# Performance work log

Measured on AMD Instinct MI355X. Metric: run time of the kernel, lower is better.

The kernel has to match this reference:

```python
import jax, jax.numpy as jnp
import numpy as np


def setup_inputs() -> dict:
    key = jax.random.key(0)
    k1, k2 = jax.random.split(key)
    B, N, C = 2, 8192, 32
    coords = jax.random.randint(k1, (B, N, 3), 0, 100, dtype=jnp.int32)
    features = jax.random.normal(k2, (B, N, C), dtype=jnp.float32)
    return {"coords": coords, "features": features, "len_batch": B}


def _detection_score(c, f):
    # c: [N,3] int32 coords, f: [N,C] float features
    f = jax.nn.relu(f)
    # beta: per-row normalization by row max
    beta = f / jnp.max(f, axis=1, keepdims=True)
    # pairwise squared distances via the exact integer expansion
    # ||a-b||^2 = |a|^2 + |b|^2 - 2 a.b  (exact in int32 for coords < 100,
    # and identical to the original's int16 arithmetic since no overflow)
    sq = jnp.sum(c * c, axis=1)                       # [N]
    d2 = sq[:, None] + sq[None, :] - 2 * (c @ c.T)    # [N,N] int32
    dist = jnp.sqrt(d2.astype(jnp.float32))           # [N,N]
    # topk(k=1, largest=False) == argmin (self-distance 0 -> nearest is self)
    nn_idx = jnp.argmin(dist, axis=1)                 # [N]
    # faithful to original: feature[neighbors,:][0] selects only row 0's
    # nearest neighbor's feature, shape [C]
    neighbor_feat = f[nn_idx[0]]                      # [C]
    alpha = jnp.exp(f) / jnp.exp(neighbor_feat)[None, :]
    gamma = jnp.max(alpha * beta, axis=1)             # [N]
    return gamma / jnp.linalg.norm(gamma)


def reference(coords, features, len_batch):
    # original concatenates per-batch scores along dim 0
    scores = jax.vmap(_detection_score)(coords, features)  # [B,N]
    return scores.reshape(-1)
```

## Files before the change

kernel.cpp:

```cpp
#include <hip/hip_runtime.h>


constexpr int kN = 8192;
constexpr int kC = 32;

__global__ __launch_bounds__(256) void gamma_kernel(const float* __restrict__ feats,
                                                    float* __restrict__ out,
                                                    float* __restrict__ sumsq) {
    const int b   = blockIdx.y;
    const int row = blockIdx.x * 256 + threadIdx.x;
    const float* fb = feats + (size_t)b * kN * kC;

    const float4* fr = reinterpret_cast<const float4*>(fb + (size_t)row * kC);
    const float4* f0 = reinterpret_cast<const float4*>(fb);

    float v[kC], r0[kC];
#pragma unroll
    for (int q = 0; q < kC / 4; ++q) {
        float4 t = fr[q];
        v[4 * q + 0] = fmaxf(t.x, 0.f);
        v[4 * q + 1] = fmaxf(t.y, 0.f);
        v[4 * q + 2] = fmaxf(t.z, 0.f);
        v[4 * q + 3] = fmaxf(t.w, 0.f);
        float4 z = f0[q];
        r0[4 * q + 0] = fmaxf(z.x, 0.f);
        r0[4 * q + 1] = fmaxf(z.y, 0.f);
        r0[4 * q + 2] = fmaxf(z.z, 0.f);
        r0[4 * q + 3] = fmaxf(z.w, 0.f);
    }

    float m = 0.f;
#pragma unroll
    for (int j = 0; j < kC; ++j) m = fmaxf(m, v[j]);
    const float inv_m = 1.0f / m;

    float g = 0.f;
#pragma unroll
    for (int j = 0; j < kC; ++j) {
        g = fmaxf(g, __expf(v[j] - r0[j]) * (v[j] * inv_m));
    }

    out[(size_t)b * kN + row] = g;

    float ss = g * g;
#pragma unroll
    for (int off = 32; off > 0; off >>= 1) ss += __shfl_down(ss, off, 64);
    if ((threadIdx.x & 63) == 0) atomicAdd(&sumsq[b], ss);
}

__global__ __launch_bounds__(256) void norm_kernel(float* __restrict__ out,
                                                   const float* __restrict__ sumsq) {
    const int i = blockIdx.x * 256 + threadIdx.x;
    const int b = i >> 13;
    out[i] = out[i] / sqrtf(sumsq[b]);
}

extern "C" void kernel_launch(void* const* d_in, const int* in_sizes, int n_in,
                              void* d_out, int out_size, void* d_ws, size_t ws_size,
                              hipStream_t stream) {
    const float* feats = (const float*)d_in[1];
    float* out = (float*)d_out;
    float* sumsq = (float*)d_ws;

    const int B = out_size / kN;

    hipMemsetAsync(sumsq, 0, (size_t)B * sizeof(float), stream);

    dim3 grid1(kN / 256, B);
    gamma_kernel<<<grid1, 256, 0, stream>>>(feats, out, sumsq);

    const int total = B * kN;
    norm_kernel<<<total / 256, 256, 0, stream>>>(out, sumsq);
}
```

Measured before the change: 64.68 us.

## Fuse gamma and normalization into one cooperative kernel with grid sync

```diff
diff --git a/kernel.cpp b/kernel.cpp
--- a/kernel.cpp
+++ b/kernel.cpp
@@ -1,74 +1,89 @@
 #include <hip/hip_runtime.h>
+#include <hip/hip_cooperative_groups.h>
+
+namespace cg = cooperative_groups;
 
 
 constexpr int kN = 8192;
 constexpr int kC = 32;
+constexpr int kBlock = 256;
+constexpr int kBlocksPerBatch = kN / kBlock;
 
-__global__ __launch_bounds__(256) void gamma_kernel(const float* __restrict__ feats,
-                                                    float* __restrict__ out,
-                                                    float* __restrict__ sumsq) {
-    const int b   = blockIdx.y;
-    const int row = blockIdx.x * 256 + threadIdx.x;
-    const float* fb = feats + (size_t)b * kN * kC;
+__global__ __launch_bounds__(kBlock) void detection_kernel(
+    const float* __restrict__ feats, float* __restrict__ out,
+    float* __restrict__ partials) {
+  cg::grid_group grid = cg::this_grid();
 
-    const float4* fr = reinterpret_cast<const float4*>(fb + (size_t)row * kC);
-    const float4* f0 = reinterpret_cast<const float4*>(fb);
+  const int blk = blockIdx.x;
+  const int b = blk / kBlocksPerBatch;
+  const int row = (blk % kBlocksPerBatch) * kBlock + threadIdx.x;
+  const float* fb = feats + (size_t)b * kN * kC;
 
-    float v[kC], r0[kC];
+  const float4* fr = reinterpret_cast<const float4*>(fb + (size_t)row * kC);
+  const float4* f0 = reinterpret_cast<const float4*>(fb);
+
+  float v[kC], r0[kC];
 #pragma unroll
-    for (int q = 0; q < kC / 4; ++q) {
-        float4 t = fr[q];
-        v[4 * q + 0] = fmaxf(t.x, 0.f);
-        v[4 * q + 1] = fmaxf(t.y, 0.f);
-        v[4 * q + 2] = fmaxf(t.z, 0.f);
-        v[4 * q + 3] = fmaxf(t.w, 0.f);
-        float4 z = f0[q];
-        r0[4 * q + 0] = fmaxf(z.x, 0.f);
-        r0[4 * q + 1] = fmaxf(z.y, 0.f);
-        r0[4 * q + 2] = fmaxf(z.z, 0.f);
-        r0[4 * q + 3] = fmaxf(z.w, 0.f);
-    }
+  for (int q = 0; q < kC / 4; ++q) {
+    float4 t = fr[q];
+    v[4 * q + 0] = fmaxf(t.x, 0.f);
+    v[4 * q + 1] = fmaxf(t.y, 0.f);
+    v[4 * q + 2] = fmaxf(t.z, 0.f);
+    v[4 * q + 3] = fmaxf(t.w, 0.f);
+    float4 z = f0[q];
+    r0[4 * q + 0] = fmaxf(z.x, 0.f);
+    r0[4 * q + 1] = fmaxf(z.y, 0.f);
+    r0[4 * q + 2] = fmaxf(z.z, 0.f);
+    r0[4 * q + 3] = fmaxf(z.w, 0.f);
+  }
 
-    float m = 0.f;
+  float m = 0.f;
 #pragma unroll
-    for (int j = 0; j < kC; ++j) m = fmaxf(m, v[j]);
-    const float inv_m = 1.0f / m;
+  for (int j = 0; j < kC; ++j) m = fmaxf(m, v[j]);
+  const float inv_m = 1.0f / m;
 
-    float g = 0.f;
+  float g = 0.f;
 #pragma unroll
-    for (int j = 0; j < kC; ++j) {
-        g = fmaxf(g, __expf(v[j] - r0[j]) * (v[j] * inv_m));
-    }
+  for (int j = 0; j < kC; ++j)
+    g = fmaxf(g, __expf(v[j] - r0[j]) * (v[j] * inv_m));
 
-    out[(size_t)b * kN + row] = g;
+  float ss = g * g;
+#pragma unroll
+  for (int off = 32; off > 0; off >>= 1) ss += __shfl_down(ss, off, 64);
+  __shared__ float s_wave[kBlock / 64];
+  if ((threadIdx.x & 63) == 0) s_wave[threadIdx.x >> 6] = ss;
+  __syncthreads();
+  if (threadIdx.x == 0)
+    partials[blk] = s_wave[0] + s_wave[1] + s_wave[2] + s_wave[3];
 
-    float ss = g * g;
+  grid.sync();
+
+  __shared__ float s_inv;
+  if (threadIdx.x < 64) {
+    float p = (threadIdx.x < kBlocksPerBatch)
+                  ? partials[b * kBlocksPerBatch + threadIdx.x]
+                  : 0.f;
 #pragma unroll
-    for (int off = 32; off > 0; off >>= 1) ss += __shfl_down(ss, off, 64);
-    if ((threadIdx.x & 63) == 0) atomicAdd(&sumsq[b], ss);
-}
+    for (int off = 16; off > 0; off >>= 1) p += __shfl_down(p, off, 64);
+    if (threadIdx.x == 0) s_inv = 1.0f / sqrtf(p);
+  }
+  __syncthreads();
 
-__global__ __launch_bounds__(256) void norm_kernel(float* __restrict__ out,
-                                                   const float* __restrict__ sumsq) {
-    const int i = blockIdx.x * 256 + threadIdx.x;
-    const int b = i >> 13;
-    out[i] = out[i] / sqrtf(sumsq[b]);
+  out[(size_t)b * kN + row] = g * s_inv;
 }
 
 extern "C" void kernel_launch(void* const* d_in, const int* in_sizes, int n_in,
-                              void* d_out, int out_size, void* d_ws, size_t ws_size,
-                              hipStream_t stream) {
-    const float* feats = (const float*)d_in[1];
-    float* out = (float*)d_out;
-    float* sumsq = (float*)d_ws;
+                              void* d_out, int out_size, void* d_ws,
+                              size_t ws_size, hipStream_t stream) {
+  const float* feats = (const float*)d_in[1];
+  float* out = (float*)d_out;
+  float* partials = (float*)d_ws;
 
-    const int B = out_size / kN;
+  const int B = out_size / kN;
+  dim3 grid(B * kBlocksPerBatch);
+  dim3 block(kBlock);
 
-    hipMemsetAsync(sumsq, 0, (size_t)B * sizeof(float), stream);
-
-    dim3 grid1(kN / 256, B);
-    gamma_kernel<<<grid1, 256, 0, stream>>>(feats, out, sumsq);
-
-    const int total = B * kN;
-    norm_kernel<<<total / 256, 256, 0, stream>>>(out, sumsq);
+  void* args[] = {(void*)&feats, (void*)&out, (void*)&partials};
+  hipLaunchCooperativeKernel((const void*)detection_kernel, grid, block, args,
+                             0, stream);
 }
```

After: 89.72 us. +38.7%, slower.
